# Performance work log

Hardware: AMD Instinct MI355X
Metric: run time of the kernel (lower is better)

Reference implementation:

```python
import jax, jax.numpy as jnp
import numpy as np

MB, E, N, IN_HALF, HID, OUT = 32, 4, 512, 64, 128, 128
EPS = 1e-5


def setup_inputs() -> dict:
    key = jax.random.key(0)
    ks = jax.random.split(key, 24)
    x = jax.random.normal(ks[0], (MB, N, IN_HALF), jnp.float32)
    u = jax.random.uniform(ks[1], (MB, E, N, N), jnp.float32)
    a = (u < 0.02).astype(jnp.float32)
    adj = jnp.maximum(a, jnp.swapaxes(a, -1, -2))  # symmetric 0/1, forward's sym branch holds
    def lin(k, i, o):
        return jax.random.normal(k, (i, o), jnp.float32) / np.float32(np.sqrt(i))
    d = {"x": x, "adj": adj}
    in_dims = [IN_HALF, HID, HID]
    for l in range(3):
        d[f"w_self{l}"] = lin(ks[2 + 6 * l], in_dims[l], HID)
        d[f"b_self{l}"] = jnp.zeros((HID,), jnp.float32)
        d[f"w_edge{l}"] = lin(ks[3 + 6 * l], in_dims[l], HID * E)
        d[f"b_edge{l}"] = jnp.zeros((HID * E,), jnp.float32)
        d[f"bn{l}_g"] = jnp.ones((N,), jnp.float32)
        d[f"bn{l}_b"] = jnp.zeros((N,), jnp.float32)
    d["w1"] = lin(ks[20], HID, HID)
    d["b1"] = jnp.zeros((HID,), jnp.float32)
    d["bn_f_g"] = jnp.ones((N,), jnp.float32)
    d["bn_f_b"] = jnp.zeros((N,), jnp.float32)
    d["w2"] = lin(ks[21], HID, OUT)
    d["b2"] = jnp.zeros((OUT,), jnp.float32)
    return d


def _rescale_adj(adj):
    # zero the diagonal, then normalize each column by total neighbor count
    n = adj.shape[-1]
    adj = adj * (1.0 - jnp.eye(n, dtype=adj.dtype))
    deg = adj.sum(axis=(1, 2))  # (mb, N): sum over edge types and rows
    inv = jnp.where(deg > 0, 1.0 / deg, 0.0)
    return inv[:, None, None, :] * adj


def _batchnorm_nodes(h, g, b):
    # torch BatchNorm1d(n_node) on (B, N, D): per-node stats over (B, D), biased var
    m = h.mean(axis=(0, 2), keepdims=True)
    v = ((h - m) ** 2).mean(axis=(0, 2), keepdims=True)
    return (h - m) / jnp.sqrt(v + EPS) * g[None, :, None] + b[None, :, None]


def _graph_conv(h, na, w_self, b_self, w_edge, b_edge):
    mb, n, _ = h.shape
    hs = h @ w_self + b_self  # (mb, N, out)
    m = (h @ w_edge + b_edge).reshape(mb, n, HID, E)  # (mb, N, out, E)
    # fused: per-edge-type adj matmul + sum over edge types, no (mb,E,N,out) blowup
    hr = jnp.einsum('benm,bmoe->bno', na, m)
    return hs + hr


def reference(x, adj,
              w_self0, b_self0, w_edge0, b_edge0, bn0_g, bn0_b,
              w_self1, b_self1, w_edge1, b_edge1, bn1_g, bn1_b,
              w_self2, b_self2, w_edge2, b_edge2, bn2_g, bn2_b,
              w1, b1, bn_f_g, bn_f_b, w2, b2):
    # adj is symmetric by construction -> forward's adj_sym == adj
    na = _rescale_adj(adj)  # identical across layers; computed once
    h = x
    layers = [
        (w_self0, b_self0, w_edge0, b_edge0, bn0_g, bn0_b),
        (w_self1, b_self1, w_edge1, b_edge1, bn1_g, bn1_b),
        (w_self2, b_self2, w_edge2, b_edge2, bn2_g, bn2_b),
    ]
    for ws, bs, we, be, g, b in layers:
        h = _graph_conv(h, na, ws, bs, we, be)
        h = _batchnorm_nodes(h, g, b)
        h = jax.nn.relu(h)
    h = h @ w1 + b1
    h = _batchnorm_nodes(h, bn_f_g, bn_f_b)
    h = jax.nn.relu(h)
    h = h @ w2 + b2
    return h
```

## Files before the change

### kernel.cpp

```cpp
#include <hip/hip_runtime.h>
#include <stdint.h>


typedef float  f32x4  __attribute__((ext_vector_type(4)));
typedef __bf16 bf16x8 __attribute__((ext_vector_type(8)));
typedef __bf16 bf16x4 __attribute__((ext_vector_type(4)));
typedef unsigned short ushort8v __attribute__((ext_vector_type(8)));
typedef uint32_t uint4v __attribute__((ext_vector_type(4)));

#define MBATCH 32
#define ETYPES 4
#define NNODE  512
#define HIDD   128

#define GLB(p) (const __attribute__((address_space(1))) uint32_t*)(p)
#define LDSp(p) (__attribute__((address_space(3))) uint32_t*)(p)

#define WP_S0 0
#define WP_E0 8192
#define WP_S1 40960
#define WP_E1 57344
#define WP_S2 122880
#define WP_E2 139264
#define WP_W1 204800
#define WP_W2 221184

__global__ __launch_bounds__(256) void k_pack(const float* __restrict__ adj,
                                              uint32_t* __restrict__ bm,
                                              float* __restrict__ degp) {
  int t = threadIdx.x;
  int wave = t >> 6, lane = t & 63;
  int r = blockIdx.x * 4 + wave;
  int b = r >> 11, e = (r >> 9) & 3, n = r & 511;
  const float* row = adj + (long)r * 512;
  uint32_t myw = 0;
#pragma unroll
  for (int i = 0; i < 8; ++i) {
    uint64_t bal = __ballot(row[i * 64 + lane] != 0.f);
    uint32_t lo = (uint32_t)bal, hi = (uint32_t)(bal >> 32);
    if ((lane >> 1) == i) myw = (lane & 1) ? hi : lo;
  }
  if (lane == (n >> 5)) myw &= ~(1u << (n & 31));
  int pc = (lane < 16) ? __popc(myw) : 0;
  pc += __shfl_down(pc, 8);
  pc += __shfl_down(pc, 4);
  pc += __shfl_down(pc, 2);
  pc += __shfl_down(pc, 1);
  if (lane < 16) bm[(long)r * 16 + lane] = myw;
  if (lane == 0) degp[e * 16384 + b * 512 + n] = (float)pc;
}

__global__ __launch_bounds__(256) void k_inv(const float* __restrict__ degp,
                                             float* __restrict__ inv) {
  int i = blockIdx.x * 256 + threadIdx.x;
  float d = degp[i] + degp[16384 + i] + degp[32768 + i] + degp[49152 + i];
  inv[i] = d > 0.f ? 1.f / d : 0.f;
}

__global__ __launch_bounds__(256) void k_prep(const float* ws0, const float* we0,
                                              const float* ws1, const float* we1,
                                              const float* ws2, const float* we2,
                                              const float* w1,  const float* w2,
                                              __bf16* __restrict__ dst) {
  int wid = blockIdx.y;
  const float* W; int K, nblk, edge, off;
  switch (wid) {
    case 0:  W = ws0; K = 64;  nblk = 2; edge = 0; off = WP_S0; break;
    case 1:  W = we0; K = 64;  nblk = 8; edge = 1; off = WP_E0; break;
    case 2:  W = ws1; K = 128; nblk = 2; edge = 0; off = WP_S1; break;
    case 3:  W = we1; K = 128; nblk = 8; edge = 1; off = WP_E1; break;
    case 4:  W = ws2; K = 128; nblk = 2; edge = 0; off = WP_S2; break;
    case 5:  W = we2; K = 128; nblk = 8; edge = 1; off = WP_E2; break;
    case 6:  W = w1;  K = 128; nblk = 2; edge = 0; off = WP_W1; break;
    default: W = w2;  K = 128; nblk = 2; edge = 0; off = WP_W2; break;
  }
  int idx = blockIdx.x * 256 + threadIdx.x;
  if (idx >= K * nblk * 64) return;
  int c = idx & 63;
  int k = (idx >> 6) % K;
  int blk = (idx >> 6) / K;
  int WS = edge ? 512 : 128;
  int col = edge ? (((blk & 1) * 64 + c) * 4 + (blk >> 1)) : (blk * 64 + c);
  dst[off + (long)blk * K * 64 + (k >> 3) * 512 + c * 8 + (k & 7)] = (__bf16)W[k * WS + col];
}

template <int K, bool F32IN>
__global__ __launch_bounds__(256) void k_gemm(const void* __restrict__ hv,
                                              const __bf16* __restrict__ wp_self,
                                              const float* __restrict__ bias_self,
                                              const __bf16* __restrict__ wp_edge,
                                              const float* __restrict__ bias_edge,
                                              const float* __restrict__ invp,
                                              float* __restrict__ outF,
                                              __bf16* __restrict__ mmp) {
  __shared__ __bf16 Hl[64][K + 8];
  __shared__ __align__(16) __bf16 Wl[K * 64];
  int t = threadIdx.x;
  int g0 = blockIdx.x * 64;
  int by = blockIdx.y;
  bool edge = by >= 2;
  int wave = t >> 6, lane = t & 63;
  {
    const __bf16* wblk = edge ? (wp_edge + (long)(by - 2) * K * 64)
                              : (wp_self + (long)by * K * 64);
    const char* g = (const char*)wblk;
#pragma unroll
    for (int i = 0; i < K / 32; ++i) {
      __builtin_amdgcn_global_load_lds(GLB(g + i * 4096 + wave * 1024 + lane * 16),
                                       LDSp((char*)Wl + i * 4096 + wave * 1024),
                                       16, 0, 0);
    }
  }
  for (int idx = t; idx < 64 * (K / 8); idx += 256) {
    int r = idx / (K / 8), ch = idx % (K / 8);
    if (F32IN) {
      const float* xf = (const float*)hv;
      f32x4 a = *(const f32x4*)(xf + (long)(g0 + r) * K + ch * 8);
      f32x4 bq = *(const f32x4*)(xf + (long)(g0 + r) * K + ch * 8 + 4);
      bf16x8 o;
#pragma unroll
      for (int j = 0; j < 4; ++j) { o[j] = (__bf16)a[j]; o[4 + j] = (__bf16)bq[j]; }
      *(bf16x8*)&Hl[r][ch * 8] = o;
    } else {
      const __bf16* hb = (const __bf16*)hv;
      *(bf16x8*)&Hl[r][ch * 8] = *(const bf16x8*)(hb + (long)(g0 + r) * K + ch * 8);
    }
  }
  __syncthreads();
  int l15 = lane & 15, q = lane >> 4;
  f32x4 acc[4] = {};
#pragma unroll
  for (int kk = 0; kk < K / 32; ++kk) {
    bf16x8 af = *(const bf16x8*)&Hl[wave * 16 + l15][kk * 32 + q * 8];
#pragma unroll
    for (int c = 0; c < 4; ++c) {
      bf16x8 bfr = *(const bf16x8*)&Wl[((kk * 4 + q) * 64 + c * 16 + l15) * 8];
      acc[c] = __builtin_amdgcn_mfma_f32_16x16x32_bf16(af, bfr, acc[c], 0, 0, 0);
    }
  }
  if (!edge) {
    int c0 = by * 64;
#pragma unroll
    for (int c = 0; c < 4; ++c) {
      float bc = bias_self[c0 + c * 16 + l15];
#pragma unroll
      for (int i = 0; i < 4; ++i) {
        int g = g0 + wave * 16 + q * 4 + i;
        outF[(long)g * HIDD + c0 + c * 16 + l15] = acc[c][i] + bc;
      }
    }
  } else {
    int blk = by - 2;
    int e = blk >> 1, o0 = (blk & 1) * 64;
    float iv[4];
#pragma unroll
    for (int i = 0; i < 4; ++i) iv[i] = invp[g0 + wave * 16 + q * 4 + i];
    int b4e  = (g0 >> 9) * 4 + e;
    int octg = ((g0 & 511) >> 3) + wave * 2 + (q >> 1);
    int j0   = (q & 1) * 4;
#pragma unroll
    for (int c = 0; c < 4; ++c) {
      int o = o0 + c * 16 + l15;
      float bc = bias_edge[o * 4 + e];
      bf16x4 v4;
#pragma unroll
      for (int i = 0; i < 4; ++i) v4[i] = (__bf16)((acc[c][i] + bc) * iv[i]);
      *(bf16x4*)(mmp + ((long)(b4e * 64 + octg) * HIDD + o) * 8 + j0) = v4;
    }
  }
}

__global__ __launch_bounds__(256) void k_spmm(const uint32_t* __restrict__ bm,
                                              const __bf16* __restrict__ mmp,
                                              float* __restrict__ part) {
  __shared__ __align__(16) __bf16 Bl[4096];
  int t = threadIdx.x;
  int bid = blockIdx.x;
  int tile = bid >> 7;
  int eb   = bid & 127;
  int e = eb >> 5, b = eb & 31;
  int nt = tile >> 1, oc = tile & 1;
  int n0 = nt * 128, o0 = oc * 64;
  int wave = t >> 6, lane = t & 63, l15 = lane & 15, q = lane >> 4;

  const uint32_t* bmr = bm + ((long)((b * 4 + e) * 512 + n0 + wave * 32 + l15)) * 16;
  uint32_t rm0[16], rm1[16];
#pragma unroll
  for (int i = 0; i < 4; ++i) {
    uint4v v0 = *(const uint4v*)(bmr + i * 4);
    uint4v v1 = *(const uint4v*)(bmr + 256 + i * 4);
    rm0[i * 4 + 0] = v0.x; rm0[i * 4 + 1] = v0.y; rm0[i * 4 + 2] = v0.z; rm0[i * 4 + 3] = v0.w;
    rm1[i * 4 + 0] = v1.x; rm1[i * 4 + 1] = v1.y; rm1[i * 4 + 2] = v1.z; rm1[i * 4 + 3] = v1.w;
  }

  f32x4 acc0[4] = {}, acc1[4] = {};
#pragma unroll 1
  for (int mc = 0; mc < 8; ++mc) {
    __syncthreads();
#pragma unroll
    for (int i = 0; i < 2; ++i) {
      int oct = wave * 2 + i;
      const char* g = (const char*)mmp +
          ((long)(b * 4 + e) * 65536 + mc * 8192 + oct * 1024 + o0 * 8) * 2;
      __builtin_amdgcn_global_load_lds(GLB(g + lane * 16),
                                       LDSp((char*)Bl + oct * 1024),
                                       16, 0, 0);
    }
    __syncthreads();
#pragma unroll
    for (int kk = 0; kk < 2; ++kk) {
      uint32_t bits0 = (rm0[mc * 2 + kk] >> (q * 8)) & 0xffu;
      uint32_t bits1 = (rm1[mc * 2 + kk] >> (q * 8)) & 0xffu;
      ushort8v a0, a1;
#pragma unroll
      for (int j = 0; j < 8; ++j) {
        a0[j] = (bits0 >> j & 1u) ? (unsigned short)0x3F80 : (unsigned short)0;
        a1[j] = (bits1 >> j & 1u) ? (unsigned short)0x3F80 : (unsigned short)0;
      }
      union { ushort8v u; bf16x8 v; } c0, c1; c0.u = a0; c1.u = a1;
#pragma unroll
      for (int c = 0; c < 4; ++c) {
        bf16x8 bfr = *(const bf16x8*)&Bl[((kk * 4 + q) * 64 + c * 16 + l15) * 8];
        acc0[c] = __builtin_amdgcn_mfma_f32_16x16x32_bf16(c0.v, bfr, acc0[c], 0, 0, 0);
        acc1[c] = __builtin_amdgcn_mfma_f32_16x16x32_bf16(c1.v, bfr, acc1[c], 0, 0, 0);
      }
    }
  }
  float* dst = part + (long)(e * 32 + b) * NNODE * HIDD;
#pragma unroll
  for (int c = 0; c < 4; ++c) {
#pragma unroll
    for (int i = 0; i < 4; ++i) {
      int n = n0 + wave * 32 + q * 4 + i;
      int o = o0 + c * 16 + l15;
      dst[(long)n * HIDD + o] = acc0[c][i];
      dst[(long)(n + 16) * HIDD + o] = acc1[c][i];
    }
  }
}

template <bool HASP>
__global__ __launch_bounds__(256) void k_bnstat(const float* __restrict__ hs,
                                                const float* __restrict__ part,
                                                const float* __restrict__ gg,
                                                const float* __restrict__ bb,
                                                __bf16* __restrict__ hb) {
  int n = blockIdx.x, t = threadIdx.x;
  int o4 = t & 31, bq = t >> 5;
  __shared__ float sm[4096];
  __shared__ float rs[256], rq[256];
  __shared__ float bc[2];
  float s = 0.f, sq = 0.f;
#pragma unroll
  for (int i = 0; i < 4; ++i) {
    int b = bq + i * 8;
    long base = ((long)b * NNODE + n) * HIDD + o4 * 4;
    f32x4 v = *(const f32x4*)(hs + base);
    if (HASP) {
#pragma unroll
      for (int e = 0; e < 4; ++e)
        v += *(const f32x4*)(part + ((long)(e * 32 + b) * NNODE + n) * HIDD + o4 * 4);
    }
    *(f32x4*)&sm[b * 128 + o4 * 4] = v;
#pragma unroll
    for (int j = 0; j < 4; ++j) { s += v[j]; sq += v[j] * v[j]; }
  }
  rs[t] = s; rq[t] = sq;
  __syncthreads();
  for (int off = 128; off > 0; off >>= 1) {
    if (t < off) { rs[t] += rs[t + off]; rq[t] += rq[t + off]; }
    __syncthreads();
  }
  if (t == 0) {
    float mean = rs[0] * (1.f / 4096.f);
    float var = rq[0] * (1.f / 4096.f) - mean * mean;
    float rstd = rsqrtf(var + 1e-5f);
    float sc = gg[n] * rstd;
    bc[0] = sc;
    bc[1] = bb[n] - mean * sc;
  }
  __syncthreads();
  float sc = bc[0], sh = bc[1];
#pragma unroll
  for (int i = 0; i < 4; ++i) {
    int b = bq + i * 8;
    f32x4 v = *(const f32x4*)&sm[b * 128 + o4 * 4];
    bf16x4 o;
#pragma unroll
    for (int j = 0; j < 4; ++j) {
      float x = v[j] * sc + sh;
      o[j] = (__bf16)(x > 0.f ? x : 0.f);
    }
    *(bf16x4*)(hb + ((long)b * NNODE + n) * HIDD + o4 * 4) = o;
  }
}

extern "C" void kernel_launch(void* const* d_in, const int* in_sizes, int n_in,
                              void* d_out, int out_size, void* d_ws, size_t ws_size,
                              hipStream_t stream) {
  (void)in_sizes; (void)n_in; (void)out_size; (void)ws_size;
  const float* x   = (const float*)d_in[0];
  const float* adj = (const float*)d_in[1];
  const float* wself[3] = {(const float*)d_in[2],  (const float*)d_in[8],  (const float*)d_in[14]};
  const float* bself[3] = {(const float*)d_in[3],  (const float*)d_in[9],  (const float*)d_in[15]};
  const float* wedge[3] = {(const float*)d_in[4],  (const float*)d_in[10], (const float*)d_in[16]};
  const float* bedge[3] = {(const float*)d_in[5],  (const float*)d_in[11], (const float*)d_in[17]};
  const float* bng[3]   = {(const float*)d_in[6],  (const float*)d_in[12], (const float*)d_in[18]};
  const float* bnb[3]   = {(const float*)d_in[7],  (const float*)d_in[13], (const float*)d_in[19]};
  const float* w1   = (const float*)d_in[20];
  const float* b1   = (const float*)d_in[21];
  const float* bnfg = (const float*)d_in[22];
  const float* bnfb = (const float*)d_in[23];
  const float* w2   = (const float*)d_in[24];
  const float* b2   = (const float*)d_in[25];

  char* ws = (char*)d_ws;
  __bf16*   mmp  = (__bf16*)ws;
  float*    hs   = (float*)(ws + 16777216);
  float*    part = (float*)(ws + 25165824);
  __bf16*   hb0  = (__bf16*)(ws + 58720256);
  __bf16*   hb1  = (__bf16*)(ws + 62914560);
  uint32_t* bm   = (uint32_t*)(ws + 67108864);
  float*    degp = (float*)(ws + 71303168);
  float*    inv  = (float*)(ws + 71565312);
  __bf16*   wp   = (__bf16*)(ws + 71630848);

  k_pack<<<16384, 256, 0, stream>>>(adj, bm, degp);
  k_inv<<<64, 256, 0, stream>>>(degp, inv);
  k_prep<<<dim3(256, 8), 256, 0, stream>>>(wself[0], wedge[0], wself[1], wedge[1],
                                           wself[2], wedge[2], w1, w2, wp);

  k_gemm<64, true><<<dim3(256, 10), 256, 0, stream>>>(x, wp + WP_S0, bself[0], wp + WP_E0,
                                                      bedge[0], inv, hs, mmp);
  k_spmm<<<1024, 256, 0, stream>>>(bm, mmp, part);
  k_bnstat<true><<<512, 256, 0, stream>>>(hs, part, bng[0], bnb[0], hb0);

  k_gemm<128, false><<<dim3(256, 10), 256, 0, stream>>>(hb0, wp + WP_S1, bself[1], wp + WP_E1,
                                                        bedge[1], inv, hs, mmp);
  k_spmm<<<1024, 256, 0, stream>>>(bm, mmp, part);
  k_bnstat<true><<<512, 256, 0, stream>>>(hs, part, bng[1], bnb[1], hb1);

  k_gemm<128, false><<<dim3(256, 10), 256, 0, stream>>>(hb1, wp + WP_S2, bself[2], wp + WP_E2,
                                                        bedge[2], inv, hs, mmp);
  k_spmm<<<1024, 256, 0, stream>>>(bm, mmp, part);
  k_bnstat<true><<<512, 256, 0, stream>>>(hs, part, bng[2], bnb[2], hb0);

  k_gemm<128, false><<<dim3(256, 2), 256, 0, stream>>>(hb0, wp + WP_W1, b1, nullptr,
                                                       nullptr, nullptr, hs, nullptr);
  k_bnstat<false><<<512, 256, 0, stream>>>(hs, nullptr, bnfg, bnfb, hb1);
  k_gemm<128, false><<<dim3(256, 2), 256, 0, stream>>>(hb1, wp + WP_W2, b2, nullptr,
                                                       nullptr, nullptr, (float*)d_out, nullptr);
}
```

Baseline: 371.2 us.

## Fuse all stages into one cooperative persistent megakernel with grid syncs

Turns the 14 separate launches into device phase functions run by a single cooperative persistent kernel, with grid-wide syncs between stages. Work is spread by grid-stride loops over tiles. The inverse degree is now computed inline in the GEMM epilogue, which removes the k_inv stage. The aim is to cut launch overhead and idle tails between stages, at the cost of grid-sync latency and occupancy limited to one resident block set. A fallback multi-launch path runs if the cooperative launch fails.

```diff
diff --git a/kernel.cpp b/kernel.cpp
--- a/kernel.cpp
+++ b/kernel.cpp
@@ -1,6 +1,9 @@
 #include <hip/hip_runtime.h>
+#include <hip/hip_cooperative_groups.h>
 #include <stdint.h>
 
+
+namespace cg = cooperative_groups;
 
 typedef float  f32x4  __attribute__((ext_vector_type(4)));
 typedef __bf16 bf16x8 __attribute__((ext_vector_type(8)));
@@ -25,329 +28,431 @@
 #define WP_W1 204800
 #define WP_W2 221184
 
-__global__ __launch_bounds__(256) void k_pack(const float* __restrict__ adj,
-                                              uint32_t* __restrict__ bm,
-                                              float* __restrict__ degp) {
-  int t = threadIdx.x;
+#define SMEM_BYTES 33792
+
+struct Params {
+  const float* x;
+  const float* adj;
+  const float* wself[3]; const float* bself[3];
+  const float* wedge[3]; const float* bedge[3];
+  const float* bng[3];   const float* bnb[3];
+  const float* w1; const float* b1;
+  const float* bnfg; const float* bnfb;
+  const float* w2; const float* b2;
+  __bf16* mmp; float* hs; float* part;
+  __bf16* hb0; __bf16* hb1;
+  uint32_t* bm; float* degp; __bf16* wp;
+  float* out;
+};
+
+__device__ void pack_phase(const float* __restrict__ adj, uint32_t* __restrict__ bm,
+                           float* __restrict__ degp, int bid, int t, int nbl) {
   int wave = t >> 6, lane = t & 63;
-  int r = blockIdx.x * 4 + wave;
-  int b = r >> 11, e = (r >> 9) & 3, n = r & 511;
-  const float* row = adj + (long)r * 512;
-  uint32_t myw = 0;
-#pragma unroll
-  for (int i = 0; i < 8; ++i) {
-    uint64_t bal = __ballot(row[i * 64 + lane] != 0.f);
-    uint32_t lo = (uint32_t)bal, hi = (uint32_t)(bal >> 32);
-    if ((lane >> 1) == i) myw = (lane & 1) ? hi : lo;
-  }
-  if (lane == (n >> 5)) myw &= ~(1u << (n & 31));
-  int pc = (lane < 16) ? __popc(myw) : 0;
-  pc += __shfl_down(pc, 8);
-  pc += __shfl_down(pc, 4);
-  pc += __shfl_down(pc, 2);
-  pc += __shfl_down(pc, 1);
-  if (lane < 16) bm[(long)r * 16 + lane] = myw;
-  if (lane == 0) degp[e * 16384 + b * 512 + n] = (float)pc;
-}
-
-__global__ __launch_bounds__(256) void k_inv(const float* __restrict__ degp,
-                                             float* __restrict__ inv) {
-  int i = blockIdx.x * 256 + threadIdx.x;
-  float d = degp[i] + degp[16384 + i] + degp[32768 + i] + degp[49152 + i];
-  inv[i] = d > 0.f ? 1.f / d : 0.f;
-}
-
-__global__ __launch_bounds__(256) void k_prep(const float* ws0, const float* we0,
-                                              const float* ws1, const float* we1,
-                                              const float* ws2, const float* we2,
-                                              const float* w1,  const float* w2,
-                                              __bf16* __restrict__ dst) {
-  int wid = blockIdx.y;
-  const float* W; int K, nblk, edge, off;
-  switch (wid) {
-    case 0:  W = ws0; K = 64;  nblk = 2; edge = 0; off = WP_S0; break;
-    case 1:  W = we0; K = 64;  nblk = 8; edge = 1; off = WP_E0; break;
-    case 2:  W = ws1; K = 128; nblk = 2; edge = 0; off = WP_S1; break;
-    case 3:  W = we1; K = 128; nblk = 8; edge = 1; off = WP_E1; break;
-    case 4:  W = ws2; K = 128; nblk = 2; edge = 0; off = WP_S2; break;
-    case 5:  W = we2; K = 128; nblk = 8; edge = 1; off = WP_E2; break;
-    case 6:  W = w1;  K = 128; nblk = 2; edge = 0; off = WP_W1; break;
-    default: W = w2;  K = 128; nblk = 2; edge = 0; off = WP_W2; break;
-  }
-  int idx = blockIdx.x * 256 + threadIdx.x;
-  if (idx >= K * nblk * 64) return;
-  int c = idx & 63;
-  int k = (idx >> 6) % K;
-  int blk = (idx >> 6) / K;
-  int WS = edge ? 512 : 128;
-  int col = edge ? (((blk & 1) * 64 + c) * 4 + (blk >> 1)) : (blk * 64 + c);
-  dst[off + (long)blk * K * 64 + (k >> 3) * 512 + c * 8 + (k & 7)] = (__bf16)W[k * WS + col];
+  for (int rg = bid; rg < 16384; rg += nbl) {
+    int r = rg * 4 + wave;
+    int b = r >> 11, e = (r >> 9) & 3, n = r & 511;
+    const float* row = adj + (long)r * 512;
+    uint32_t myw = 0;
+#pragma unroll
+    for (int i = 0; i < 8; ++i) {
+      uint64_t bal = __ballot(row[i * 64 + lane] != 0.f);
+      uint32_t lo = (uint32_t)bal, hi = (uint32_t)(bal >> 32);
+      if ((lane >> 1) == i) myw = (lane & 1) ? hi : lo;
+    }
+    if (lane == (n >> 5)) myw &= ~(1u << (n & 31));
+    int pc = (lane < 16) ? __popc(myw) : 0;
+    pc += __shfl_down(pc, 8);
+    pc += __shfl_down(pc, 4);
+    pc += __shfl_down(pc, 2);
+    pc += __shfl_down(pc, 1);
+    if (lane < 16) bm[(long)r * 16 + lane] = myw;
+    if (lane == 0) degp[e * 16384 + b * 512 + n] = (float)pc;
+  }
+}
+
+__device__ void prep_phase(const Params& P, int bid, int t, int nbl) {
+  const float* Ws[8] = {P.wself[0], P.wedge[0], P.wself[1], P.wedge[1],
+                        P.wself[2], P.wedge[2], P.w1, P.w2};
+  const int Kt[8]  = {64, 64, 128, 128, 128, 128, 128, 128};
+  const int NB[8]  = {2, 8, 2, 8, 2, 8, 2, 2};
+  const int OFF[8] = {WP_S0, WP_E0, WP_S1, WP_E1, WP_S2, WP_E2, WP_W1, WP_W2};
+#pragma unroll
+  for (int wid = 0; wid < 8; ++wid) {
+    int K = Kt[wid], nblk = NB[wid];
+    int tot = K * nblk * 64;
+    for (int gid = bid * 256 + t; gid < tot; gid += nbl * 256) {
+      int c = gid & 63;
+      int k = (gid >> 6) % K;
+      int blk = (gid >> 6) / K;
+      int edge = (nblk == 8);
+      int WS = edge ? 512 : 128;
+      int col = edge ? (((blk & 1) * 64 + c) * 4 + (blk >> 1)) : (blk * 64 + c);
+      P.wp[OFF[wid] + (long)blk * K * 64 + (k >> 3) * 512 + c * 8 + (k & 7)] =
+          (__bf16)Ws[wid][k * WS + col];
+    }
+  }
 }
 
 template <int K, bool F32IN>
-__global__ __launch_bounds__(256) void k_gemm(const void* __restrict__ hv,
-                                              const __bf16* __restrict__ wp_self,
-                                              const float* __restrict__ bias_self,
-                                              const __bf16* __restrict__ wp_edge,
-                                              const float* __restrict__ bias_edge,
-                                              const float* __restrict__ invp,
-                                              float* __restrict__ outF,
-                                              __bf16* __restrict__ mmp) {
-  __shared__ __bf16 Hl[64][K + 8];
-  __shared__ __align__(16) __bf16 Wl[K * 64];
-  int t = threadIdx.x;
-  int g0 = blockIdx.x * 64;
-  int by = blockIdx.y;
-  bool edge = by >= 2;
-  int wave = t >> 6, lane = t & 63;
-  {
-    const __bf16* wblk = edge ? (wp_edge + (long)(by - 2) * K * 64)
-                              : (wp_self + (long)by * K * 64);
-    const char* g = (const char*)wblk;
-#pragma unroll
-    for (int i = 0; i < K / 32; ++i) {
-      __builtin_amdgcn_global_load_lds(GLB(g + i * 4096 + wave * 1024 + lane * 16),
-                                       LDSp((char*)Wl + i * 4096 + wave * 1024),
-                                       16, 0, 0);
-    }
-  }
-  for (int idx = t; idx < 64 * (K / 8); idx += 256) {
-    int r = idx / (K / 8), ch = idx % (K / 8);
-    if (F32IN) {
-      const float* xf = (const float*)hv;
-      f32x4 a = *(const f32x4*)(xf + (long)(g0 + r) * K + ch * 8);
-      f32x4 bq = *(const f32x4*)(xf + (long)(g0 + r) * K + ch * 8 + 4);
-      bf16x8 o;
-#pragma unroll
-      for (int j = 0; j < 4; ++j) { o[j] = (__bf16)a[j]; o[4 + j] = (__bf16)bq[j]; }
-      *(bf16x8*)&Hl[r][ch * 8] = o;
+__device__ void gemm_phase(char* smem, const void* __restrict__ hv,
+                           const __bf16* __restrict__ wp_self,
+                           const float* __restrict__ bias_self,
+                           const __bf16* __restrict__ wp_edge,
+                           const float* __restrict__ bias_edge,
+                           const float* __restrict__ degp,
+                           float* __restrict__ outF, __bf16* __restrict__ mmp,
+                           int ntiles, int bid, int t, int nbl) {
+  __bf16 (*Hl)[K + 8] = (__bf16(*)[K + 8])smem;
+  __bf16* Wl = (__bf16*)(smem + 64 * (K + 8) * 2);
+  int wave = t >> 6, lane = t & 63, l15 = lane & 15, q = lane >> 4;
+  for (int tile = bid; tile < ntiles; tile += nbl) {
+    __syncthreads();
+    int g0 = (tile & 255) * 64;
+    int by = tile >> 8;
+    bool edge = by >= 2;
+    {
+      const __bf16* wblk = edge ? (wp_edge + (long)(by - 2) * K * 64)
+                                : (wp_self + (long)by * K * 64);
+      const char* g = (const char*)wblk;
+#pragma unroll
+      for (int i = 0; i < K / 32; ++i) {
+        __builtin_amdgcn_global_load_lds(GLB(g + i * 4096 + wave * 1024 + lane * 16),
+                                         LDSp((char*)Wl + i * 4096 + wave * 1024),
+                                         16, 0, 0);
+      }
+    }
+    for (int idx = t; idx < 64 * (K / 8); idx += 256) {
+      int r = idx / (K / 8), ch = idx % (K / 8);
+      if (F32IN) {
+        const float* xf = (const float*)hv;
+        f32x4 a = *(const f32x4*)(xf + (long)(g0 + r) * K + ch * 8);
+        f32x4 bq = *(const f32x4*)(xf + (long)(g0 + r) * K + ch * 8 + 4);
+        bf16x8 o;
+#pragma unroll
+        for (int j = 0; j < 4; ++j) { o[j] = (__bf16)a[j]; o[4 + j] = (__bf16)bq[j]; }
+        *(bf16x8*)&Hl[r][ch * 8] = o;
+      } else {
+        const __bf16* hb = (const __bf16*)hv;
+        *(bf16x8*)&Hl[r][ch * 8] = *(const bf16x8*)(hb + (long)(g0 + r) * K + ch * 8);
+      }
+    }
+    __syncthreads();
+    f32x4 acc[4] = {};
+#pragma unroll
+    for (int kk = 0; kk < K / 32; ++kk) {
+      bf16x8 af = *(const bf16x8*)&Hl[wave * 16 + l15][kk * 32 + q * 8];
+#pragma unroll
+      for (int c = 0; c < 4; ++c) {
+        bf16x8 bfr = *(const bf16x8*)&Wl[((kk * 4 + q) * 64 + c * 16 + l15) * 8];
+        acc[c] = __builtin_amdgcn_mfma_f32_16x16x32_bf16(af, bfr, acc[c], 0, 0, 0);
+      }
+    }
+    if (!edge) {
+      int c0 = by * 64;
+#pragma unroll
+      for (int c = 0; c < 4; ++c) {
+        float bc = bias_self[c0 + c * 16 + l15];
+#pragma unroll
+        for (int i = 0; i < 4; ++i) {
+          int g = g0 + wave * 16 + q * 4 + i;
+          outF[(long)g * HIDD + c0 + c * 16 + l15] = acc[c][i] + bc;
+        }
+      }
     } else {
-      const __bf16* hb = (const __bf16*)hv;
-      *(bf16x8*)&Hl[r][ch * 8] = *(const bf16x8*)(hb + (long)(g0 + r) * K + ch * 8);
-    }
-  }
-  __syncthreads();
-  int l15 = lane & 15, q = lane >> 4;
-  f32x4 acc[4] = {};
-#pragma unroll
-  for (int kk = 0; kk < K / 32; ++kk) {
-    bf16x8 af = *(const bf16x8*)&Hl[wave * 16 + l15][kk * 32 + q * 8];
+      int blk = by - 2;
+      int e = blk >> 1, o0 = (blk & 1) * 64;
+      float iv[4];
+#pragma unroll
+      for (int i = 0; i < 4; ++i) {
+        int gg = g0 + wave * 16 + q * 4 + i;
+        float d = degp[gg] + degp[16384 + gg] + degp[32768 + gg] + degp[49152 + gg];
+        iv[i] = d > 0.f ? 1.f / d : 0.f;
+      }
+      int b4e  = (g0 >> 9) * 4 + e;
+      int octg = ((g0 & 511) >> 3) + wave * 2 + (q >> 1);
+      int j0   = (q & 1) * 4;
+#pragma unroll
+      for (int c = 0; c < 4; ++c) {
+        int o = o0 + c * 16 + l15;
+        float bc = bias_edge[o * 4 + e];
+        bf16x4 v4;
+#pragma unroll
+        for (int i = 0; i < 4; ++i) v4[i] = (__bf16)((acc[c][i] + bc) * iv[i]);
+        *(bf16x4*)(mmp + ((long)(b4e * 64 + octg) * HIDD + o) * 8 + j0) = v4;
+      }
+    }
+  }
+}
+
+__device__ void spmm_phase(char* smem, const uint32_t* __restrict__ bm,
+                           const __bf16* __restrict__ mmp,
+                           float* __restrict__ part, int bid, int t, int nbl) {
+  __bf16* Bl = (__bf16*)smem;
+  int wave = t >> 6, lane = t & 63, l15 = lane & 15, q = lane >> 4;
+  for (int tl = bid; tl < 1024; tl += nbl) {
+    int tile = tl >> 7;
+    int eb   = tl & 127;
+    int e = eb >> 5, b = eb & 31;
+    int nt = tile >> 1, oc = tile & 1;
+    int n0 = nt * 128, o0 = oc * 64;
+
+    const uint32_t* bmr = bm + ((long)((b * 4 + e) * 512 + n0 + wave * 32 + l15)) * 16;
+    uint32_t rm0[16], rm1[16];
+#pragma unroll
+    for (int i = 0; i < 4; ++i) {
+      uint4v v0 = *(const uint4v*)(bmr + i * 4);
+      uint4v v1 = *(const uint4v*)(bmr + 256 + i * 4);
+      rm0[i * 4 + 0] = v0.x; rm0[i * 4 + 1] = v0.y; rm0[i * 4 + 2] = v0.z; rm0[i * 4 + 3] = v0.w;
+      rm1[i * 4 + 0] = v1.x; rm1[i * 4 + 1] = v1.y; rm1[i * 4 + 2] = v1.z; rm1[i * 4 + 3] = v1.w;
+    }
+
+    f32x4 acc0[4] = {}, acc1[4] = {};
+#pragma unroll 1
+    for (int mc = 0; mc < 8; ++mc) {
+      __syncthreads();
+#pragma unroll
+      for (int i = 0; i < 2; ++i) {
+        int oct = wave * 2 + i;
+        const char* g = (const char*)mmp +
+            ((long)(b * 4 + e) * 65536 + mc * 8192 + oct * 1024 + o0 * 8) * 2;
+        __builtin_amdgcn_global_load_lds(GLB(g + lane * 16),
+                                         LDSp((char*)Bl + oct * 1024),
+                                         16, 0, 0);
+      }
+      __syncthreads();
+#pragma unroll
+      for (int kk = 0; kk < 2; ++kk) {
+        uint32_t bits0 = (rm0[mc * 2 + kk] >> (q * 8)) & 0xffu;
+        uint32_t bits1 = (rm1[mc * 2 + kk] >> (q * 8)) & 0xffu;
+        ushort8v a0, a1;
+#pragma unroll
+        for (int j = 0; j < 8; ++j) {
+          a0[j] = (bits0 >> j & 1u) ? (unsigned short)0x3F80 : (unsigned short)0;
+          a1[j] = (bits1 >> j & 1u) ? (unsigned short)0x3F80 : (unsigned short)0;
+        }
+        union { ushort8v u; bf16x8 v; } c0, c1; c0.u = a0; c1.u = a1;
+#pragma unroll
+        for (int c = 0; c < 4; ++c) {
+          bf16x8 bfr = *(const bf16x8*)&Bl[((kk * 4 + q) * 64 + c * 16 + l15) * 8];
+          acc0[c] = __builtin_amdgcn_mfma_f32_16x16x32_bf16(c0.v, bfr, acc0[c], 0, 0, 0);
+          acc1[c] = __builtin_amdgcn_mfma_f32_16x16x32_bf16(c1.v, bfr, acc1[c], 0, 0, 0);
+        }
+      }
+    }
+    float* dst = part + (long)(e * 32 + b) * NNODE * HIDD;
 #pragma unroll
     for (int c = 0; c < 4; ++c) {
-      bf16x8 bfr = *(const bf16x8*)&Wl[((kk * 4 + q) * 64 + c * 16 + l15) * 8];
-      acc[c] = __builtin_amdgcn_mfma_f32_16x16x32_bf16(af, bfr, acc[c], 0, 0, 0);
-    }
-  }
-  if (!edge) {
-    int c0 = by * 64;
-#pragma unroll
-    for (int c = 0; c < 4; ++c) {
-      float bc = bias_self[c0 + c * 16 + l15];
 #pragma unroll
       for (int i = 0; i < 4; ++i) {
-        int g = g0 + wave * 16 + q * 4 + i;
-        outF[(long)g * HIDD + c0 + c * 16 + l15] = acc[c][i] + bc;
-      }
-    }
-  } else {
-    int blk = by - 2;
-    int e = blk >> 1, o0 = (blk & 1) * 64;
-    float iv[4];
-#pragma unroll
-    for (int i = 0; i < 4; ++i) iv[i] = invp[g0 + wave * 16 + q * 4 + i];
-    int b4e  = (g0 >> 9) * 4 + e;
-    int octg = ((g0 & 511) >> 3) + wave * 2 + (q >> 1);
-    int j0   = (q & 1) * 4;
-#pragma unroll
-    for (int c = 0; c < 4; ++c) {
-      int o = o0 + c * 16 + l15;
-      float bc = bias_edge[o * 4 + e];
-      bf16x4 v4;
-#pragma unroll
-      for (int i = 0; i < 4; ++i) v4[i] = (__bf16)((acc[c][i] + bc) * iv[i]);
-      *(bf16x4*)(mmp + ((long)(b4e * 64 + octg) * HIDD + o) * 8 + j0) = v4;
-    }
-  }
-}
-
-__global__ __launch_bounds__(256) void k_spmm(const uint32_t* __restrict__ bm,
-                                              const __bf16* __restrict__ mmp,
-                                              float* __restrict__ part) {
-  __shared__ __align__(16) __bf16 Bl[4096];
-  int t = threadIdx.x;
-  int bid = blockIdx.x;
-  int tile = bid >> 7;
-  int eb   = bid & 127;
-  int e = eb >> 5, b = eb & 31;
-  int nt = tile >> 1, oc = tile & 1;
-  int n0 = nt * 128, o0 = oc * 64;
-  int wave = t >> 6, lane = t & 63, l15 = lane & 15, q = lane >> 4;
-
-  const uint32_t* bmr = bm + ((long)((b * 4 + e) * 512 + n0 + wave * 32 + l15)) * 16;
-  uint32_t rm0[16], rm1[16];
-#pragma unroll
-  for (int i = 0; i < 4; ++i) {
-    uint4v v0 = *(const uint4v*)(bmr + i * 4);
-    uint4v v1 = *(const uint4v*)(bmr + 256 + i * 4);
-    rm0[i * 4 + 0] = v0.x; rm0[i * 4 + 1] = v0.y; rm0[i * 4 + 2] = v0.z; rm0[i * 4 + 3] = v0.w;
-    rm1[i * 4 + 0] = v1.x; rm1[i * 4 + 1] = v1.y; rm1[i * 4 + 2] = v1.z; rm1[i * 4 + 3] = v1.w;
-  }
-
-  f32x4 acc0[4] = {}, acc1[4] = {};
-#pragma unroll 1
-  for (int mc = 0; mc < 8; ++mc) {
+        int n = n0 + wave * 32 + q * 4 + i;
+        int o = o0 + c * 16 + l15;
+        dst[(long)n * HIDD + o] = acc0[c][i];
+        dst[(long)(n + 16) * HIDD + o] = acc1[c][i];
+      }
+    }
+  }
+}
+
+template <bool HASP>
+__device__ void bnstat_phase(char* smem, const float* __restrict__ hs,
+                             const float* __restrict__ part,
+                             const float* __restrict__ gg,
+                             const float* __restrict__ bb,
+                             __bf16* __restrict__ hb, int bid, int t, int nbl) {
+  float* sm = (float*)smem;
+  float* rs = (float*)(smem + 16384);
+  float* rq = (float*)(smem + 17408);
+  float* bc = (float*)(smem + 18432);
+  int o4 = t & 31, bq = t >> 5;
+  for (int n = bid; n < 512; n += nbl) {
     __syncthreads();
-#pragma unroll
-    for (int i = 0; i < 2; ++i) {
-      int oct = wave * 2 + i;
-      const char* g = (const char*)mmp +
-          ((long)(b * 4 + e) * 65536 + mc * 8192 + oct * 1024 + o0 * 8) * 2;
-      __builtin_amdgcn_global_load_lds(GLB(g + lane * 16),
-                                       LDSp((char*)Bl + oct * 1024),
-                                       16, 0, 0);
-    }
+    float s = 0.f, sq = 0.f;
+#pragma unroll
+    for (int i = 0; i < 4; ++i) {
+      int b = bq + i * 8;
+      long base = ((long)b * NNODE + n) * HIDD + o4 * 4;
+      f32x4 v = *(const f32x4*)(hs + base);
+      if (HASP) {
+#pragma unroll
+        for (int e = 0; e < 4; ++e)
+          v += *(const f32x4*)(part + ((long)(e * 32 + b) * NNODE + n) * HIDD + o4 * 4);
+      }
+      *(f32x4*)&sm[b * 128 + o4 * 4] = v;
+#pragma unroll
+      for (int j = 0; j < 4; ++j) { s += v[j]; sq += v[j] * v[j]; }
+    }
+    rs[t] = s; rq[t] = sq;
     __syncthreads();
-#pragma unroll
-    for (int kk = 0; kk < 2; ++kk) {
-      uint32_t bits0 = (rm0[mc * 2 + kk] >> (q * 8)) & 0xffu;
-      uint32_t bits1 = (rm1[mc * 2 + kk] >> (q * 8)) & 0xffu;
-      ushort8v a0, a1;
-#pragma unroll
-      for (int j = 0; j < 8; ++j) {
-        a0[j] = (bits0 >> j & 1u) ? (unsigned short)0x3F80 : (unsigned short)0;
-        a1[j] = (bits1 >> j & 1u) ? (unsigned short)0x3F80 : (unsigned short)0;
-      }
-      union { ushort8v u; bf16x8 v; } c0, c1; c0.u = a0; c1.u = a1;
-#pragma unroll
-      for (int c = 0; c < 4; ++c) {
-        bf16x8 bfr = *(const bf16x8*)&Bl[((kk * 4 + q) * 64 + c * 16 + l15) * 8];
-        acc0[c] = __builtin_amdgcn_mfma_f32_16x16x32_bf16(c0.v, bfr, acc0[c], 0, 0, 0);
-        acc1[c] = __builtin_amdgcn_mfma_f32_16x16x32_bf16(c1.v, bfr, acc1[c], 0, 0, 0);
-      }
-    }
-  }
-  float* dst = part + (long)(e * 32 + b) * NNODE * HIDD;
-#pragma unroll
-  for (int c = 0; c < 4; ++c) {
+    for (int off = 128; off > 0; off >>= 1) {
+      if (t < off) { rs[t] += rs[t + off]; rq[t] += rq[t + off]; }
+      __syncthreads();
+    }
+    if (t == 0) {
+      float mean = rs[0] * (1.f / 4096.f);
+      float var = rq[0] * (1.f / 4096.f) - mean * mean;
+      float rstd = rsqrtf(var + 1e-5f);
+      float sc = gg[n] * rstd;
+      bc[0] = sc;
+      bc[1] = bb[n] - mean * sc;
+    }
+    __syncthreads();
+    float sc = bc[0], sh = bc[1];
 #pragma unroll
     for (int i = 0; i < 4; ++i) {
-      int n = n0 + wave * 32 + q * 4 + i;
-      int o = o0 + c * 16 + l15;
-      dst[(long)n * HIDD + o] = acc0[c][i];
-      dst[(long)(n + 16) * HIDD + o] = acc1[c][i];
-    }
-  }
-}
-
+      int b = bq + i * 8;
+      f32x4 v = *(const f32x4*)&sm[b * 128 + o4 * 4];
+      bf16x4 o;
+#pragma unroll
+      for (int j = 0; j < 4; ++j) {
+        float x = v[j] * sc + sh;
+        o[j] = (__bf16)(x > 0.f ? x : 0.f);
+      }
+      *(bf16x4*)(hb + ((long)b * NNODE + n) * HIDD + o4 * 4) = o;
+    }
+  }
+}
+
+__global__ __launch_bounds__(256, 4) void k_mega(Params P) {
+  cg::grid_group grid = cg::this_grid();
+  __shared__ __align__(16) char smem[SMEM_BYTES];
+  int bid = blockIdx.x, t = threadIdx.x, nbl = gridDim.x;
+
+  pack_phase(P.adj, P.bm, P.degp, bid, t, nbl);
+  prep_phase(P, bid, t, nbl);
+  grid.sync();
+
+  gemm_phase<64, true>(smem, P.x, P.wp + WP_S0, P.bself[0], P.wp + WP_E0,
+                       P.bedge[0], P.degp, P.hs, P.mmp, 2560, bid, t, nbl);
+  grid.sync();
+  spmm_phase(smem, P.bm, P.mmp, P.part, bid, t, nbl);
+  grid.sync();
+  bnstat_phase<true>(smem, P.hs, P.part, P.bng[0], P.bnb[0], P.hb0, bid, t, nbl);
+  grid.sync();
+
+  gemm_phase<128, false>(smem, P.hb0, P.wp + WP_S1, P.bself[1], P.wp + WP_E1,
+                         P.bedge[1], P.degp, P.hs, P.mmp, 2560, bid, t, nbl);
+  grid.sync();
+  spmm_phase(smem, P.bm, P.mmp, P.part, bid, t, nbl);
+  grid.sync();
+  bnstat_phase<true>(smem, P.hs, P.part, P.bng[1], P.bnb[1], P.hb1, bid, t, nbl);
+  grid.sync();
+
+  gemm_phase<128, false>(smem, P.hb1, P.wp + WP_S2, P.bself[2], P.wp + WP_E2,
+                         P.bedge[2], P.degp, P.hs, P.mmp, 2560, bid, t, nbl);
+  grid.sync();
+  spmm_phase(smem, P.bm, P.mmp, P.part, bid, t, nbl);
+  grid.sync();
+  bnstat_phase<true>(smem, P.hs, P.part, P.bng[2], P.bnb[2], P.hb0, bid, t, nbl);
+  grid.sync();
+
+  gemm_phase<128, false>(smem, P.hb0, P.wp + WP_W1, P.b1, nullptr,
+                         nullptr, P.degp, P.hs, nullptr, 512, bid, t, nbl);
+  grid.sync();
+  bnstat_phase<false>(smem, P.hs, nullptr, P.bnfg, P.bnfb, P.hb1, bid, t, nbl);
+  grid.sync();
+  gemm_phase<128, false>(smem, P.hb1, P.wp + WP_W2, P.b2, nullptr,
+                         nullptr, P.degp, P.out, nullptr, 512, bid, t, nbl);
+}
+
+__global__ __launch_bounds__(256) void g_packprep(Params P) {
+  pack_phase(P.adj, P.bm, P.degp, blockIdx.x, threadIdx.x, gridDim.x);
+  prep_phase(P, blockIdx.x, threadIdx.x, gridDim.x);
+}
+template <int K, bool F32IN>
+__global__ __launch_bounds__(256) void g_gemm(const void* hv, const __bf16* wps,
+                                              const float* bs, const __bf16* wpe,
+                                              const float* be, const float* degp,
+                                              float* outF, __bf16* mmp, int ntiles) {
+  __shared__ __align__(16) char smem[64 * (K + 8) * 2 + K * 64 * 2];
+  gemm_phase<K, F32IN>(smem, hv, wps, bs, wpe, be, degp, outF, mmp, ntiles,
+                       blockIdx.x, threadIdx.x, gridDim.x);
+}
+__global__ __launch_bounds__(256) void g_spmm(const uint32_t* bm, const __bf16* mmp,
+                                              float* part) {
+  __shared__ __align__(16) char smem[8192];
+  spmm_phase(smem, bm, mmp, part, blockIdx.x, threadIdx.x, gridDim.x);
+}
 template <bool HASP>
-__global__ __launch_bounds__(256) void k_bnstat(const float* __restrict__ hs,
-                                                const float* __restrict__ part,
-                                                const float* __restrict__ gg,
-                                                const float* __restrict__ bb,
-                                                __bf16* __restrict__ hb) {
-  int n = blockIdx.x, t = threadIdx.x;
-  int o4 = t & 31, bq = t >> 5;
-  __shared__ float sm[4096];
-  __shared__ float rs[256], rq[256];
-  __shared__ float bc[2];
-  float s = 0.f, sq = 0.f;
-#pragma unroll
-  for (int i = 0; i < 4; ++i) {
-    int b = bq + i * 8;
-    long base = ((long)b * NNODE + n) * HIDD + o4 * 4;
-    f32x4 v = *(const f32x4*)(hs + base);
-    if (HASP) {
-#pragma unroll
-      for (int e = 0; e < 4; ++e)
-        v += *(const f32x4*)(part + ((long)(e * 32 + b) * NNODE + n) * HIDD + o4 * 4);
-    }
-    *(f32x4*)&sm[b * 128 + o4 * 4] = v;
-#pragma unroll
-    for (int j = 0; j < 4; ++j) { s += v[j]; sq += v[j] * v[j]; }
-  }
-  rs[t] = s; rq[t] = sq;
-  __syncthreads();
-  for (int off = 128; off > 0; off >>= 1) {
-    if (t < off) { rs[t] += rs[t + off]; rq[t] += rq[t + off]; }
-    __syncthreads();
-  }
-  if (t == 0) {
-    float mean = rs[0] * (1.f / 4096.f);
-    float var = rq[0] * (1.f / 4096.f) - mean * mean;
-    float rstd = rsqrtf(var + 1e-5f);
-    float sc = gg[n] * rstd;
-    bc[0] = sc;
-    bc[1] = bb[n] - mean * sc;
-  }
-  __syncthreads();
-  float sc = bc[0], sh = bc[1];
-#pragma unroll
-  for (int i = 0; i < 4; ++i) {
-    int b = bq + i * 8;
-    f32x4 v = *(const f32x4*)&sm[b * 128 + o4 * 4];
-    bf16x4 o;
-#pragma unroll
-    for (int j = 0; j < 4; ++j) {
-      float x = v[j] * sc + sh;
-      o[j] = (__bf16)(x > 0.f ? x : 0.f);
-    }
-    *(bf16x4*)(hb + ((long)b * NNODE + n) * HIDD + o4 * 4) = o;
-  }
+__global__ __launch_bounds__(256) void g_bnstat(const float* hs, const float* part,
+                                                const float* gg, const float* bb,
+                                                __bf16* hb) {
+  __shared__ __align__(16) char smem[18448];
+  bnstat_phase<HASP>(smem, hs, part, gg, bb, hb, blockIdx.x, threadIdx.x, gridDim.x);
 }
 
 extern "C" void kernel_launch(void* const* d_in, const int* in_sizes, int n_in,
                               void* d_out, int out_size, void* d_ws, size_t ws_size,
                               hipStream_t stream) {
   (void)in_sizes; (void)n_in; (void)out_size; (void)ws_size;
-  const float* x   = (const float*)d_in[0];
-  const float* adj = (const float*)d_in[1];
-  const float* wself[3] = {(const float*)d_in[2],  (const float*)d_in[8],  (const float*)d_in[14]};
-  const float* bself[3] = {(const float*)d_in[3],  (const float*)d_in[9],  (const float*)d_in[15]};
-  const float* wedge[3] = {(const float*)d_in[4],  (const float*)d_in[10], (const float*)d_in[16]};
-  const float* bedge[3] = {(const float*)d_in[5],  (const float*)d_in[11], (const float*)d_in[17]};
-  const float* bng[3]   = {(const float*)d_in[6],  (const float*)d_in[12], (const float*)d_in[18]};
-  const float* bnb[3]   = {(const float*)d_in[7],  (const float*)d_in[13], (const float*)d_in[19]};
-  const float* w1   = (const float*)d_in[20];
-  const float* b1   = (const float*)d_in[21];
-  const float* bnfg = (const float*)d_in[22];
-  const float* bnfb = (const float*)d_in[23];
-  const float* w2   = (const float*)d_in[24];
-  const float* b2   = (const float*)d_in[25];
+  Params P;
+  P.x   = (const float*)d_in[0];
+  P.adj = (const float*)d_in[1];
+  for (int l = 0; l < 3; ++l) {
+    P.wself[l] = (const float*)d_in[2 + 6 * l];
+    P.bself[l] = (const float*)d_in[3 + 6 * l];
+    P.wedge[l] = (const float*)d_in[4 + 6 * l];
+    P.bedge[l] = (const float*)d_in[5 + 6 * l];
+    P.bng[l]   = (const float*)d_in[6 + 6 * l];
+    P.bnb[l]   = (const float*)d_in[7 + 6 * l];
+  }
+  P.w1   = (const float*)d_in[20];
+  P.b1   = (const float*)d_in[21];
+  P.bnfg = (const float*)d_in[22];
+  P.bnfb = (const float*)d_in[23];
+  P.w2   = (const float*)d_in[24];
+  P.b2   = (const float*)d_in[25];
 
   char* ws = (char*)d_ws;
-  __bf16*   mmp  = (__bf16*)ws;
-  float*    hs   = (float*)(ws + 16777216);
-  float*    part = (float*)(ws + 25165824);
-  __bf16*   hb0  = (__bf16*)(ws + 58720256);
-  __bf16*   hb1  = (__bf16*)(ws + 62914560);
-  uint32_t* bm   = (uint32_t*)(ws + 67108864);
-  float*    degp = (float*)(ws + 71303168);
-  float*    inv  = (float*)(ws + 71565312);
-  __bf16*   wp   = (__bf16*)(ws + 71630848);
-
-  k_pack<<<16384, 256, 0, stream>>>(adj, bm, degp);
-  k_inv<<<64, 256, 0, stream>>>(degp, inv);
-  k_prep<<<dim3(256, 8), 256, 0, stream>>>(wself[0], wedge[0], wself[1], wedge[1],
-                                           wself[2], wedge[2], w1, w2, wp);
-
-  k_gemm<64, true><<<dim3(256, 10), 256, 0, stream>>>(x, wp + WP_S0, bself[0], wp + WP_E0,
-                                                      bedge[0], inv, hs, mmp);
-  k_spmm<<<1024, 256, 0, stream>>>(bm, mmp, part);
-  k_bnstat<true><<<512, 256, 0, stream>>>(hs, part, bng[0], bnb[0], hb0);
-
-  k_gemm<128, false><<<dim3(256, 10), 256, 0, stream>>>(hb0, wp + WP_S1, bself[1], wp + WP_E1,
-                                                        bedge[1], inv, hs, mmp);
-  k_spmm<<<1024, 256, 0, stream>>>(bm, mmp, part);
-  k_bnstat<true><<<512, 256, 0, stream>>>(hs, part, bng[1], bnb[1], hb1);
-
-  k_gemm<128, false><<<dim3(256, 10), 256, 0, stream>>>(hb1, wp + WP_S2, bself[2], wp + WP_E2,
-                                                        bedge[2], inv, hs, mmp);
-  k_spmm<<<1024, 256, 0, stream>>>(bm, mmp, part);
-  k_bnstat<true><<<512, 256, 0, stream>>>(hs, part, bng[2], bnb[2], hb0);
-
-  k_gemm<128, false><<<dim3(256, 2), 256, 0, stream>>>(hb0, wp + WP_W1, b1, nullptr,
-                                                       nullptr, nullptr, hs, nullptr);
-  k_bnstat<false><<<512, 256, 0, stream>>>(hs, nullptr, bnfg, bnfb, hb1);
-  k_gemm<128, false><<<dim3(256, 2), 256, 0, stream>>>(hb1, wp + WP_W2, b2, nullptr,
-                                                       nullptr, nullptr, (float*)d_out, nullptr);
-}
+  P.mmp  = (__bf16*)ws;
+  P.hs   = (float*)(ws + 16777216);
+  P.part = (float*)(ws + 25165824);
+  P.hb0  = (__bf16*)(ws + 58720256);
+  P.hb1  = (__bf16*)(ws + 62914560);
+  P.bm   = (uint32_t*)(ws + 67108864);
+  P.degp = (float*)(ws + 71303168);
+  P.wp   = (__bf16*)(ws + 71565312);
+  P.out  = (float*)d_out;
+
+  int dev = 0;
+  hipGetDevice(&dev);
+  int ncu = 256;
+  hipDeviceGetAttribute(&ncu, hipDeviceAttributeMultiprocessorCount, dev);
+  int coop = 0;
+  hipDeviceGetAttribute(&coop, hipDeviceAttributeCooperativeLaunch, dev);
+  int nb = 0;
+  hipOccupancyMaxActiveBlocksPerMultiprocessor(&nb, k_mega, 256, 0);
+
+  hipError_t err = hipErrorUnknown;
+  if (coop && nb >= 1) {
+    long grid = (long)nb * ncu;
+    if (grid > 1024) grid = 1024;
+    void* args[] = {(void*)&P};
+    err = hipLaunchCooperativeKernel((const void*)k_mega, dim3((uint32_t)grid),
+                                     dim3(256), args, 0, stream);
+  }
+  if (err != hipSuccess) {
+    g_packprep<<<1024, 256, 0, stream>>>(P);
+    g_gemm<64, true><<<1024, 256, 0, stream>>>(P.x, P.wp + WP_S0, P.bself[0],
+                                               P.wp + WP_E0, P.bedge[0], P.degp,
+                                               P.hs, P.mmp, 2560);
+    g_spmm<<<1024, 256, 0, stream>>>(P.bm, P.mmp, P.part);
+    g_bnstat<true><<<512, 256, 0, stream>>>(P.hs, P.part, P.bng[0], P.bnb[0], P.hb0);
+    g_gemm<128, false><<<1024, 256, 0, stream>>>(P.hb0, P.wp + WP_S1, P.bself[1],
+                                                 P.wp + WP_E1, P.bedge[1], P.degp,
+                                                 P.hs, P.mmp, 2560);
+    g_spmm<<<1024, 256, 0, stream>>>(P.bm, P.mmp, P.part);
+    g_bnstat<true><<<512, 256, 0, stream>>>(P.hs, P.part, P.bng[1], P.bnb[1], P.hb1);
+    g_gemm<128, false><<<1024, 256, 0, stream>>>(P.hb1, P.wp + WP_S2, P.bself[2],
+                                                 P.wp + WP_E2, P.bedge[2], P.degp,
+                                                 P.hs, P.mmp, 2560);
+    g_spmm<<<1024, 256, 0, stream>>>(P.bm, P.mmp, P.part);
+    g_bnstat<true><<<512, 256, 0, stream>>>(P.hs, P.part, P.bng[2], P.bnb[2], P.hb0);
+    g_gemm<128, false><<<512, 256, 0, stream>>>(P.hb0, P.wp + WP_W1, P.b1,
+                                                nullptr, nullptr, P.degp,
+                                                P.hs, nullptr, 512);
+    g_bnstat<false><<<512, 256, 0, stream>>>(P.hs, nullptr, P.bnfg, P.bnfb, P.hb1);
+    g_gemm<128, false><<<512, 256, 0, stream>>>(P.hb1, P.wp + WP_W2, P.b2,
+                                                nullptr, nullptr, P.degp,
+                                                P.out, nullptr, 512);
+  }
+}
```

Result: slower. 1.144 ms (+208.2%).
